# Kernel tuning notes

Measured on AMD Instinct MI355X. Metric: run time of the kernel, lower is better.

## Reference

```python
import jax, jax.numpy as jnp
import numpy as np

B, S, T = 128, 2048, 128


def setup_inputs() -> dict:
    key = jax.random.key(0)
    k1, k2, k3, k4, k5, k6 = jax.random.split(key, 6)
    logit = jax.random.normal(k1, (B, S, T), jnp.float32)
    target = jax.random.randint(k2, (B, S), 0, T, dtype=jnp.int32)
    seq_lens = jax.random.randint(k3, (B,), 1, S + 1, dtype=jnp.int32)
    transitions = 0.1 * jax.random.normal(k4, (T, T), jnp.float32)
    start_transitions = 0.1 * jax.random.normal(k5, (T,), jnp.float32)
    end_transitions = 0.1 * jax.random.normal(k6, (T,), jnp.float32)
    return dict(logit=logit, target=target, seq_lens=seq_lens,
                transitions=transitions, start_transitions=start_transitions,
                end_transitions=end_transitions)


def reference(logit, target, seq_lens, transitions, start_transitions, end_transitions):
    # logit: [B,S,T] batch-first; CRF works time-first like the torch code's transpose(0,1)
    em = jnp.transpose(logit, (1, 0, 2))          # [S,B,T]
    tg = target.T                                  # [S,B]
    mask = jnp.arange(S)[:, None] < seq_lens[None, :]  # [S,B]

    # ---- loss: -mean log-likelihood (CRF forward algorithm) ----
    emit = jnp.take_along_axis(em, tg[..., None], -1)[..., 0]   # [S,B]
    trans_sc = transitions[tg[:-1], tg[1:]]                      # [S-1,B]
    num = start_transitions[tg[0]] + emit[0]
    num = num + jnp.sum(jnp.where(mask[1:], emit[1:] + trans_sc, 0.0), axis=0)
    last_tags = jnp.take_along_axis(tg, (seq_lens - 1)[None, :], 0)[0]  # [B]
    num = num + end_transitions[last_tags]

    def fstep(alpha, xs):
        e_t, m_t = xs  # [B,T], [B]
        nxt = jax.nn.logsumexp(alpha[:, :, None] + transitions[None] + e_t[:, None, :], axis=1)
        return jnp.where(m_t[:, None], nxt, alpha), None

    alpha0 = start_transitions[None, :] + em[0]   # [B,T]
    alpha, _ = jax.lax.scan(fstep, alpha0, (em[1:], mask[1:]))
    logZ = jax.nn.logsumexp(alpha + end_transitions[None, :], axis=-1)  # [B]
    loss = -(num - logZ).mean()

    # ---- Viterbi decode ----
    tag_ids = jnp.arange(T, dtype=jnp.int32)

    def vstep(score, xs):
        e_t, m_t = xs
        mat = score[:, :, None] + transitions[None] + e_t[:, None, :]  # [B,Tprev,Tcur]
        best = mat.max(axis=1)
        idx = mat.argmax(axis=1).astype(jnp.int32)
        score = jnp.where(m_t[:, None], best, score)
        idx = jnp.where(m_t[:, None], idx, tag_ids[None, :])  # identity beyond seq end
        return score, idx

    vscore, hist = jax.lax.scan(vstep, alpha0, (em[1:], mask[1:]))  # hist: [S-1,B,T]
    last_tag = jnp.argmax(vscore + end_transitions[None, :], axis=-1).astype(jnp.int32)

    def bstep(tag, idx_t):
        prev = jnp.take_along_axis(idx_t, tag[:, None], 1)[:, 0]
        return prev, prev

    _, tags_prev = jax.lax.scan(bstep, last_tag, hist, reverse=True)  # [S-1,B]
    pred = jnp.concatenate([tags_prev, last_tag[None, :]], axis=0).T  # [B,S]

    # ---- _rearrange_output: swap decoded-tag logit with the max logit ----
    maxidx = jnp.argmax(logit, axis=-1)                         # [B,S]
    maxval = jnp.max(logit, axis=-1)                            # [B,S]
    vval = jnp.take_along_axis(logit, pred[..., None], -1)[..., 0]  # [B,S]
    oh_v = pred[..., None] == tag_ids[None, None, :]
    oh_m = maxidx[..., None] == tag_ids[None, None, :]
    swapped = jnp.where(oh_v, maxval[..., None],
                        jnp.where(oh_m, vval[..., None], logit))
    log_probs = jax.nn.log_softmax(swapped, axis=-1)            # [B,S,T]

    return loss, pred, log_probs
```

## Files before the change

kernel.cpp:

```cpp
#include <hip/hip_runtime.h>
#include <stdint.h>

#define BB 128
#define SS 2048
#define TT 128
#define NSEG 32
#define SEGK 64

#define TRP 129
#define VSTRIDE 136
#define H1OFF 68

typedef float f32x4 __attribute__((ext_vector_type(4)));

#define BAR() asm volatile("s_waitcnt lgkmcnt(0)\n\ts_barrier" ::: "memory")

#define PIN(x) asm volatile("" : "+v"(x))

__device__ __forceinline__ float dpp_swap1_f(float x) {
    int i = __float_as_int(x);
    i = __builtin_amdgcn_update_dpp(0, i, 0xB1, 0xF, 0xF, true);
    return __int_as_float(i);
}
__device__ __forceinline__ int dpp_swap1_i(int x) {
    return __builtin_amdgcn_update_dpp(0, x, 0xB1, 0xF, 0xF, true);
}

__attribute__((amdgpu_flat_work_group_size(256, 256)))
__attribute__((amdgpu_waves_per_eu(1, 1)))
__global__ void crf_mainX(const float* __restrict__ logit,
                          const int* __restrict__ seq_lens,
                          const float* __restrict__ trans,
                          const float* __restrict__ startT,
                          const float* __restrict__ endT,
                          const int* __restrict__ target,
                          uint8_t* __restrict__ histG,
                          float* __restrict__ scr_logZ,
                          int* __restrict__ scr_last,
                          float* __restrict__ scr_num)
{
    extern __shared__ float smem[];
    float* transLDS = smem;
    float* vecLDS   = smem + 16512;
    float* ringLDS  = smem + 16512 + 272;
    float* redLDS   = smem + 16512 + 276;
    int*   redILDS  = (int*)(smem + 16512 + 284);
    float* sumLDS   = smem + 16512 + 288;

    const int bid = blockIdx.x;
    const int role = bid >> 7;
    const int b = bid & (BB - 1);
    const int tid = threadIdx.x;
    const int j = tid >> 1;
    const int h = tid & 1;
    const int ibase0 = h << 6;
    const int joff = j + ((j >= 64) ? (H1OFF - 64) : 0);
    const int L = seq_lens[b];
    const size_t lbase = (size_t)b * (SS * TT);

    for (int m = tid; m < TT * TT; m += 256)
        transLDS[(m >> 7) * TRP + (m & 127)] = trans[m];
    __syncthreads();

    float e1 = 0.f, e2 = 0.f, e3 = 0.f;
    if (L > 1) e1 = logit[lbase + TT + j];
    e2 = (L > 2) ? logit[lbase + 2 * (size_t)TT + j] : e1;
    e3 = (L > 3) ? logit[lbase + 3 * (size_t)TT + j] : e2;

    if (role == 0) {
        f32x4 tC[16];
#pragma unroll
        for (int c = 0; c < 16; ++c) {
            tC[c].x = transLDS[(ibase0 + c * 4 + 0) * TRP + j];
            tC[c].y = transLDS[(ibase0 + c * 4 + 1) * TRP + j];
            tC[c].z = transLDS[(ibase0 + c * 4 + 2) * TRP + j];
            tC[c].w = transLDS[(ibase0 + c * 4 + 3) * TRP + j];
            PIN(tC[c]);
        }
        const float a0 = startT[j] + logit[lbase + j];
        if (h == 0) vecLDS[joff] = a0;
        __syncthreads();

        for (int t = 1; t < L; ++t) {
            const int cur = (t - 1) & 1, nxt = t & 1;
            const float e = e1; e1 = e2; e2 = e3;
            const int tn = (t + 3 < L) ? (t + 3) : (L - 1);
            e3 = logit[lbase + (size_t)tn * TT + j];

            const f32x4* sq = (const f32x4*)(vecLDS + cur * VSTRIDE + h * H1OFF);
            float cm[8];
#pragma unroll
            for (int c = 0; c < 8; ++c) {
                f32x4 pa = sq[2 * c] + tC[2 * c];
                f32x4 pb = sq[2 * c + 1] + tC[2 * c + 1];
                float m01 = fmaxf(pa.x, pa.y), m23 = fmaxf(pa.z, pa.w);
                float m45 = fmaxf(pb.x, pb.y), m67 = fmaxf(pb.z, pb.w);
                cm[c] = fmaxf(fmaxf(m01, m23), fmaxf(m45, m67));
            }
            float M = fmaxf(fmaxf(fmaxf(cm[0], cm[1]), fmaxf(cm[2], cm[3])),
                            fmaxf(fmaxf(cm[4], cm[5]), fmaxf(cm[6], cm[7])));
            const float Mall = fmaxf(M, dpp_swap1_f(M));
            const float v = Mall + e;

            int cwin = -1;
#pragma unroll
            for (int c = 7; c >= 0; --c) cwin = ((cm[c] + e) == v) ? c : cwin;

            int idx = 0x7fffffff;
            if (cwin >= 0) {
                const int basei = ibase0 + cwin * 8;
                const float* tr = transLDS + (size_t)basei * TRP + j;
                const f32x4* sr = (const f32x4*)(vecLDS + cur * VSTRIDE + h * H1OFF + cwin * 8);
                f32x4 ra = sr[0], rb = sr[1];
                float q0 = (ra.x + tr[0 * TRP]) + e;
                float q1 = (ra.y + tr[1 * TRP]) + e;
                float q2 = (ra.z + tr[2 * TRP]) + e;
                float q3 = (ra.w + tr[3 * TRP]) + e;
                float q4 = (rb.x + tr[4 * TRP]) + e;
                float q5 = (rb.y + tr[5 * TRP]) + e;
                float q6 = (rb.z + tr[6 * TRP]) + e;
                float q7 = (rb.w + tr[7 * TRP]) + e;
                idx = (q7 == v) ? basei + 7 : idx;
                idx = (q6 == v) ? basei + 6 : idx;
                idx = (q5 == v) ? basei + 5 : idx;
                idx = (q4 == v) ? basei + 4 : idx;
                idx = (q3 == v) ? basei + 3 : idx;
                idx = (q2 == v) ? basei + 2 : idx;
                idx = (q1 == v) ? basei + 1 : idx;
                idx = (q0 == v) ? basei + 0 : idx;
            }
            const int oidx = dpp_swap1_i(idx);
            idx = (oidx < idx) ? oidx : idx;

            if (h == 0) {
                vecLDS[nxt * VSTRIDE + joff] = v;
                histG[(size_t)b * (SS * TT) + (size_t)t * TT + j] = (uint8_t)idx;
            }
            BAR();
        }

        const int fin = (L - 1) & 1;
        if (tid < 128) {
            const int toff = tid + ((tid >= 64) ? (H1OFF - 64) : 0);
            float lv = vecLDS[fin * VSTRIDE + toff] + endT[tid];
            int li = tid;
#pragma unroll
            for (int off = 1; off < 64; off <<= 1) {
                float ov = __shfl_xor(lv, off);
                int oi = __shfl_xor(li, off);
                if (ov > lv || (ov == lv && oi < li)) { lv = ov; li = oi; }
            }
            if ((tid & 63) == 0) { redLDS[tid >> 6] = lv; redILDS[tid >> 6] = li; }
        }
        __syncthreads();
        if (tid == 0) {
            int lt = (redLDS[1] > redLDS[0] ||
                      (redLDS[1] == redLDS[0] && redILDS[1] < redILDS[0]))
                     ? redILDS[1] : redILDS[0];
            scr_last[b] = lt;
        }
        uint8_t* hb = histG + (size_t)b * (SS * TT);
        const int colq = (tid & 7) * 16;
        const uint32_t w0 = 0x03020100u + 0x01010101u * (uint32_t)colq;
        const uint4 pat = make_uint4(w0, w0 + 0x04040404u, w0 + 0x08080808u, w0 + 0x0C0C0C0Cu);
        for (int t0 = L; t0 < SS; t0 += 32) {
            int t = t0 + (tid >> 3);
            if (t < SS) *(uint4*)(hb + (size_t)t * TT + colq) = pat;
        }
    } else {
        f32x4 tE[16];
#pragma unroll
        for (int c = 0; c < 16; ++c) {
            tE[c].x = __expf(transLDS[(ibase0 + c * 4 + 0) * TRP + j]);
            tE[c].y = __expf(transLDS[(ibase0 + c * 4 + 1) * TRP + j]);
            tE[c].z = __expf(transLDS[(ibase0 + c * 4 + 2) * TRP + j]);
            tE[c].w = __expf(transLDS[(ibase0 + c * 4 + 3) * TRP + j]);
            PIN(tE[c]);
        }
        const float a0 = startT[j] + logit[lbase + j];
        const float R0 = startT[0] + logit[lbase + 0];
        float alpha = a0;
        if (h == 0) vecLDS[joff] = __expf(a0 - R0);
        if (tid < 4) ringLDS[tid] = R0;
        __syncthreads();

        for (int t = 1; t < L; ++t) {
            const int cur = (t - 1) & 1, nxt = t & 1;
            const float Rcons = ringLDS[(t - 3) & 3];
            const float Rpub  = ringLDS[(t - 2) & 3];
            const float e = e1; e1 = e2; e2 = e3;
            const int tn = (t + 3 < L) ? (t + 3) : (L - 1);
            e3 = logit[lbase + (size_t)tn * TT + j];

            const f32x4* aq = (const f32x4*)(vecLDS + cur * VSTRIDE + h * H1OFF);
            f32x4 s4 = {0.f, 0.f, 0.f, 0.f};
            f32x4 s4b = {0.f, 0.f, 0.f, 0.f};
#pragma unroll
            for (int c = 0; c < 16; c += 2) {
                s4  = aq[c] * tE[c] + s4;
                s4b = aq[c + 1] * tE[c + 1] + s4b;
            }
            f32x4 st = s4 + s4b;
            float Ssum = (st.x + st.y) + (st.z + st.w);
            Ssum += dpp_swap1_f(Ssum);
            alpha = e + Rcons + __logf(Ssum);
            const float p = __expf(alpha - Rpub);
            if (h == 0) vecLDS[nxt * VSTRIDE + joff] = p;
            if (tid == 0) ringLDS[t & 3] = alpha;
            BAR();
        }

        const float fval = alpha + endT[j];
        float tmx = fval;
#pragma unroll
        for (int off = 1; off < 64; off <<= 1) tmx = fmaxf(tmx, __shfl_xor(tmx, off));
        if ((tid & 63) == 0) redLDS[4 + (tid >> 6)] = tmx;
        __syncthreads();
        const float gm = fmaxf(fmaxf(redLDS[4], redLDS[5]), fmaxf(redLDS[6], redLDS[7]));
        float se = (h == 0) ? __expf(fval - gm) : 0.f;
#pragma unroll
        for (int off = 1; off < 64; off <<= 1) se += __shfl_xor(se, off);
        if ((tid & 63) == 0) sumLDS[tid >> 6] = se;
        __syncthreads();
        if (tid == 0)
            scr_logZ[b] = gm + __logf(sumLDS[0] + sumLDS[1] + sumLDS[2] + sumLDS[3]);
        __syncthreads();

        float acc = 0.f;
        for (int t = tid; t < L; t += 256) {
            int tg = target[b * SS + t];
            acc += logit[((size_t)b * SS + t) * TT + tg];
            if (t >= 1) acc += trans[target[b * SS + t - 1] * TT + tg];
        }
#pragma unroll
        for (int off = 1; off < 64; off <<= 1) acc += __shfl_xor(acc, off);
        if ((tid & 63) == 0) sumLDS[tid >> 6] = acc;
        __syncthreads();
        if (tid == 0) {
            float tot = sumLDS[0] + sumLDS[1] + sumLDS[2] + sumLDS[3];
            tot += startT[target[b * SS]] + endT[target[b * SS + L - 1]];
            scr_num[b] = tot;
        }
    }
}

__global__ void crf_btseg(uint8_t* __restrict__ histG)
{
    const int c = blockIdx.x;
    const int b = blockIdx.y;
    const int tid = threadIdx.x;
    __shared__ __align__(16) uint8_t hl[SEGK * TT];

    const int lo = (c == 0) ? 1 : c * SEGK;
    const int nr = (c == 0) ? 63 : 64;
    const uint8_t* src = histG + (size_t)b * (SS * TT) + (size_t)lo * TT;
    for (int k = tid; k < (nr * TT) / 16; k += 128)
        ((uint4*)hl)[k] = ((const uint4*)src)[k];
    __syncthreads();

    int tau = tid;
    uint32_t w[16];
#pragma unroll
    for (int q = 0; q < 16; ++q) w[q] = 0u;
    if (c == 0) {
#pragma unroll
        for (int r = 62; r >= 0; --r) {
            tau = hl[r * TT + tau];
            w[r >> 2] |= ((uint32_t)tau) << ((r & 3) * 8);
        }
    } else {
#pragma unroll
        for (int r = 63; r >= 0; --r) {
            tau = hl[r * TT + tau];
            w[r >> 2] |= ((uint32_t)tau) << ((r & 3) * 8);
        }
    }
    uint4* dst = (uint4*)(histG + (size_t)b * (SS * TT) + (size_t)c * 8192 + (size_t)tid * 64);
    dst[0] = make_uint4(w[0], w[1], w[2], w[3]);
    dst[1] = make_uint4(w[4], w[5], w[6], w[7]);
    dst[2] = make_uint4(w[8], w[9], w[10], w[11]);
    dst[3] = make_uint4(w[12], w[13], w[14], w[15]);
}

__global__ void crf_btchain(const uint8_t* __restrict__ histG,
                            const int* __restrict__ scr_last,
                            int* __restrict__ scr_bt,
                            float* __restrict__ out_pred)
{
    const int b = threadIdx.x;
    if (b >= BB) return;
    int tau = scr_last[b];
    out_pred[(size_t)b * SS + (SS - 1)] = (float)tau;
    for (int c = NSEG - 1; c >= 0; --c) {
        scr_bt[b * NSEG + c] = tau;
        tau = histG[(size_t)b * (SS * TT) + (size_t)c * 8192 + (size_t)tau * 64];
    }
}

__global__ void crf_btfill(const uint8_t* __restrict__ histG,
                           const int* __restrict__ scr_bt,
                           float* __restrict__ out_pred)
{
    const int c = blockIdx.x;
    const int b = blockIdx.y;
    const int s = threadIdx.x;
    if (c == 0 && s > 62) return;
    const int js = scr_bt[b * NSEG + c];
    uint8_t v = histG[(size_t)b * (SS * TT) + (size_t)c * 8192 + (size_t)js * 64 + s];
    const int pos = (c == 0) ? s : (c * SEGK - 1 + s);
    out_pred[(size_t)b * SS + pos] = (float)v;
}

__global__ void crf_loss(const float* __restrict__ scr_logZ, const float* __restrict__ scr_num,
                         float* __restrict__ out)
{
    const int tid = threadIdx.x;
    __shared__ float p2[2];
    float v = (tid < BB) ? (scr_logZ[tid] - scr_num[tid]) : 0.0f;
#pragma unroll
    for (int off = 1; off < 64; off <<= 1) v += __shfl_xor(v, off);
    if ((tid & 63) == 0) p2[tid >> 6] = v;
    __syncthreads();
    if (tid == 0) out[0] = (p2[0] + p2[1]) / (float)BB;
}

__global__ void crf_logprobs(const float* __restrict__ logit,
                             const float* __restrict__ predF,
                             float* __restrict__ outLP)
{
    const int wid = threadIdx.x >> 6;
    const int lane = threadIdx.x & 63;
    const size_t row = (size_t)blockIdx.x * 4 + wid;
    const float2* rp = (const float2*)(logit + row * TT);
    float2 v = rp[lane];
    const int pred = (int)predF[row];

    float mv; int mi;
    if (v.y > v.x) { mv = v.y; mi = lane * 2 + 1; }
    else           { mv = v.x; mi = lane * 2; }
#pragma unroll
    for (int off = 1; off < 64; off <<= 1) {
        float ov = __shfl_xor(mv, off);
        int oi = __shfl_xor(mi, off);
        if (ov > mv || (ov == mv && oi < mi)) { mv = ov; mi = oi; }
    }
    float se = __expf(v.x - mv) + __expf(v.y - mv);
#pragma unroll
    for (int off = 1; off < 64; off <<= 1) se += __shfl_xor(se, off);
    const float lse = __logf(se);

    float px = __shfl(v.x, pred >> 1);
    float py = __shfl(v.y, pred >> 1);
    float vp = (pred & 1) ? py : px;

    float ox = (lane * 2 == pred) ? mv : ((lane * 2 == mi) ? vp : v.x);
    float oy = (lane * 2 + 1 == pred) ? mv : ((lane * 2 + 1 == mi) ? vp : v.y);
    float* op = outLP + row * TT + lane * 2;
    op[0] = (ox - mv) - lse;
    op[1] = (oy - mv) - lse;
}

extern "C" void kernel_launch(void* const* d_in, const int* in_sizes, int n_in,
                              void* d_out, int out_size, void* d_ws, size_t ws_size,
                              hipStream_t stream)
{
    const float* logit    = (const float*)d_in[0];
    const int*   target   = (const int*)d_in[1];
    const int*   seq_lens = (const int*)d_in[2];
    const float* trans    = (const float*)d_in[3];
    const float* startT   = (const float*)d_in[4];
    const float* endT     = (const float*)d_in[5];

    float* out      = (float*)d_out;
    float* out_pred = out + 1;
    float* outLP    = out + 1 + (size_t)BB * SS;
    uint8_t* histG  = (uint8_t*)(out + 262148);
    float* scr      = out + ((size_t)1 + (size_t)BB * SS + (size_t)BB * SS * TT - 4480);
    float* scr_logZ = scr;
    float* scr_num  = scr + 128;
    int*   scr_last = (int*)(scr + 256);
    int*   scr_bt   = (int*)(scr + 384);

    const int dynLDS = (16512 + 272 + 4 + 8 + 4 + 4 + 8) * 4;
    hipFuncSetAttribute((const void*)crf_mainX,
                        hipFuncAttributeMaxDynamicSharedMemorySize, dynLDS);

    crf_mainX<<<2 * BB, 256, dynLDS, stream>>>(logit, seq_lens, trans, startT, endT,
                                               target, histG, scr_logZ, scr_last, scr_num);
    crf_btseg<<<dim3(NSEG, BB), 128, 0, stream>>>(histG);
    crf_btchain<<<1, 128, 0, stream>>>(histG, scr_last, scr_bt, out_pred);
    crf_btfill<<<dim3(NSEG, BB), 64, 0, stream>>>(histG, scr_bt, out_pred);
    crf_loss<<<1, 128, 0, stream>>>(scr_logZ, scr_num, out);
    crf_logprobs<<<(BB * SS) / 4, 256, 0, stream>>>(logit, out_pred, outLP);
}
```

Measured before the change: 1.591 ms.

## Remap CRF recurrence threads to 4 outputs x 8 input groups per lane

Changes the thread mapping in the forward and Viterbi recurrences. Each lane now computes 4 output tags over a 16-wide slice of previous tags, where before it handled one tag over half the inputs. The 8-lane reduction uses three DPP steps, and emissions, state writes and history bytes move as 4-wide vectors. The goal is to cut LDS state reads per step and vectorize the global accesses, at the cost of a longer DPP reduction chain per step and a new padded state layout.

```diff
diff --git a/kernel.cpp b/kernel.cpp
--- a/kernel.cpp
+++ b/kernel.cpp
@@ -8,22 +8,28 @@
 #define SEGK 64
 
 #define TRP 129
-#define VSTRIDE 136
-#define H1OFF 68
+#define SPITCH 160
+#define PI(i) ((i) + (((i) >> 4) << 2))
 
 typedef float f32x4 __attribute__((ext_vector_type(4)));
 
 #define BAR() asm volatile("s_waitcnt lgkmcnt(0)\n\ts_barrier" ::: "memory")
-
 #define PIN(x) asm volatile("" : "+v"(x))
 
-__device__ __forceinline__ float dpp_swap1_f(float x) {
-    int i = __float_as_int(x);
-    i = __builtin_amdgcn_update_dpp(0, i, 0xB1, 0xF, 0xF, true);
-    return __int_as_float(i);
-}
-__device__ __forceinline__ int dpp_swap1_i(int x) {
-    return __builtin_amdgcn_update_dpp(0, x, 0xB1, 0xF, 0xF, true);
+template <int CTRL>
+__device__ __forceinline__ float dppf(float x) {
+    return __int_as_float(__builtin_amdgcn_update_dpp(0, __float_as_int(x), CTRL, 0xF, 0xF, true));
+}
+template <int CTRL>
+__device__ __forceinline__ int dppi(int x) {
+    return __builtin_amdgcn_update_dpp(0, x, CTRL, 0xF, 0xF, true);
+}
+
+__device__ __forceinline__ f32x4 fmax4(f32x4 a, f32x4 b) {
+    f32x4 r;
+    r.x = fmaxf(a.x, b.x); r.y = fmaxf(a.y, b.y);
+    r.z = fmaxf(a.z, b.z); r.w = fmaxf(a.w, b.w);
+    return r;
 }
 
 __attribute__((amdgpu_flat_work_group_size(256, 256)))
@@ -41,20 +47,22 @@
 {
     extern __shared__ float smem[];
     float* transLDS = smem;
-    float* vecLDS   = smem + 16512;
-    float* ringLDS  = smem + 16512 + 272;
-    float* redLDS   = smem + 16512 + 276;
-    int*   redILDS  = (int*)(smem + 16512 + 284);
-    float* sumLDS   = smem + 16512 + 288;
-
-    const int bid = blockIdx.x;
+    float* stateLDS = smem + 16512;
+    float* ringLDS  = smem + 16832;
+    float* redLDS   = smem + 16836;
+    int*   redILDS  = (int*)(smem + 16844);
+    float* sumLDS   = smem + 16848;
+
+    const int bid  = blockIdx.x;
     const int role = bid >> 7;
-    const int b = bid & (BB - 1);
-    const int tid = threadIdx.x;
-    const int j = tid >> 1;
-    const int h = tid & 1;
-    const int ibase0 = h << 6;
-    const int joff = j + ((j >= 64) ? (H1OFF - 64) : 0);
+    const int b    = bid & (BB - 1);
+    const int tid  = threadIdx.x;
+    const int w    = tid >> 6;
+    const int lane = tid & 63;
+    const int ig   = lane & 7;
+    const int jd   = lane >> 3;
+    const int j0   = w * 32 + jd * 4;
+    const int ibase = ig * 16;
     const int L = seq_lens[b];
     const size_t lbase = (size_t)b * (SS * TT);
 
@@ -62,87 +70,89 @@
         transLDS[(m >> 7) * TRP + (m & 127)] = trans[m];
     __syncthreads();
 
-    float e1 = 0.f, e2 = 0.f, e3 = 0.f;
-    if (L > 1) e1 = logit[lbase + TT + j];
-    e2 = (L > 2) ? logit[lbase + 2 * (size_t)TT + j] : e1;
-    e3 = (L > 3) ? logit[lbase + 3 * (size_t)TT + j] : e2;
+    f32x4 e1 = {0,0,0,0}, e2, e3;
+    if (L > 1) e1 = *(const f32x4*)(logit + lbase + (size_t)TT + j0);
+    e2 = (L > 2) ? *(const f32x4*)(logit + lbase + 2 * (size_t)TT + j0) : e1;
+    e3 = (L > 3) ? *(const f32x4*)(logit + lbase + 3 * (size_t)TT + j0) : e2;
+
+    const f32x4 st4 = *(const f32x4*)(startT + j0);
+    const f32x4 l04 = *(const f32x4*)(logit + lbase + j0);
+    const f32x4 a04 = st4 + l04;
 
     if (role == 0) {
-        f32x4 tC[16];
-#pragma unroll
-        for (int c = 0; c < 16; ++c) {
-            tC[c].x = transLDS[(ibase0 + c * 4 + 0) * TRP + j];
-            tC[c].y = transLDS[(ibase0 + c * 4 + 1) * TRP + j];
-            tC[c].z = transLDS[(ibase0 + c * 4 + 2) * TRP + j];
-            tC[c].w = transLDS[(ibase0 + c * 4 + 3) * TRP + j];
-            PIN(tC[c]);
-        }
-        const float a0 = startT[j] + logit[lbase + j];
-        if (h == 0) vecLDS[joff] = a0;
-        __syncthreads();
+        f32x4 tj[4][4];
+#pragma unroll
+        for (int q = 0; q < 4; ++q)
+#pragma unroll
+            for (int c = 0; c < 4; ++c) {
+                tj[q][c].x = transLDS[(ibase + c * 4 + 0) * TRP + (j0 + q)];
+                tj[q][c].y = transLDS[(ibase + c * 4 + 1) * TRP + (j0 + q)];
+                tj[q][c].z = transLDS[(ibase + c * 4 + 2) * TRP + (j0 + q)];
+                tj[q][c].w = transLDS[(ibase + c * 4 + 3) * TRP + (j0 + q)];
+                PIN(tj[q][c]);
+            }
+        if (ig == 0) *(f32x4*)(stateLDS + PI(j0)) = a04;
+        __syncthreads();
+
+        uint8_t* hb = histG + (size_t)b * (SS * TT);
 
         for (int t = 1; t < L; ++t) {
             const int cur = (t - 1) & 1, nxt = t & 1;
-            const float e = e1; e1 = e2; e2 = e3;
+            const f32x4 e4 = e1; e1 = e2; e2 = e3;
             const int tn = (t + 3 < L) ? (t + 3) : (L - 1);
-            e3 = logit[lbase + (size_t)tn * TT + j];
-
-            const f32x4* sq = (const f32x4*)(vecLDS + cur * VSTRIDE + h * H1OFF);
-            float cm[8];
-#pragma unroll
-            for (int c = 0; c < 8; ++c) {
-                f32x4 pa = sq[2 * c] + tC[2 * c];
-                f32x4 pb = sq[2 * c + 1] + tC[2 * c + 1];
-                float m01 = fmaxf(pa.x, pa.y), m23 = fmaxf(pa.z, pa.w);
-                float m45 = fmaxf(pb.x, pb.y), m67 = fmaxf(pb.z, pb.w);
-                cm[c] = fmaxf(fmaxf(m01, m23), fmaxf(m45, m67));
-            }
-            float M = fmaxf(fmaxf(fmaxf(cm[0], cm[1]), fmaxf(cm[2], cm[3])),
-                            fmaxf(fmaxf(cm[4], cm[5]), fmaxf(cm[6], cm[7])));
-            const float Mall = fmaxf(M, dpp_swap1_f(M));
-            const float v = Mall + e;
-
-            int cwin = -1;
-#pragma unroll
-            for (int c = 7; c >= 0; --c) cwin = ((cm[c] + e) == v) ? c : cwin;
-
-            int idx = 0x7fffffff;
-            if (cwin >= 0) {
-                const int basei = ibase0 + cwin * 8;
-                const float* tr = transLDS + (size_t)basei * TRP + j;
-                const f32x4* sr = (const f32x4*)(vecLDS + cur * VSTRIDE + h * H1OFF + cwin * 8);
-                f32x4 ra = sr[0], rb = sr[1];
-                float q0 = (ra.x + tr[0 * TRP]) + e;
-                float q1 = (ra.y + tr[1 * TRP]) + e;
-                float q2 = (ra.z + tr[2 * TRP]) + e;
-                float q3 = (ra.w + tr[3 * TRP]) + e;
-                float q4 = (rb.x + tr[4 * TRP]) + e;
-                float q5 = (rb.y + tr[5 * TRP]) + e;
-                float q6 = (rb.z + tr[6 * TRP]) + e;
-                float q7 = (rb.w + tr[7 * TRP]) + e;
-                idx = (q7 == v) ? basei + 7 : idx;
-                idx = (q6 == v) ? basei + 6 : idx;
-                idx = (q5 == v) ? basei + 5 : idx;
-                idx = (q4 == v) ? basei + 4 : idx;
-                idx = (q3 == v) ? basei + 3 : idx;
-                idx = (q2 == v) ? basei + 2 : idx;
-                idx = (q1 == v) ? basei + 1 : idx;
-                idx = (q0 == v) ? basei + 0 : idx;
-            }
-            const int oidx = dpp_swap1_i(idx);
-            idx = (oidx < idx) ? oidx : idx;
-
-            if (h == 0) {
-                vecLDS[nxt * VSTRIDE + joff] = v;
-                histG[(size_t)b * (SS * TT) + (size_t)t * TT + j] = (uint8_t)idx;
+            e3 = *(const f32x4*)(logit + lbase + (size_t)tn * TT + j0);
+
+            const f32x4* sq = (const f32x4*)(stateLDS + cur * SPITCH + 20 * ig);
+            f32x4 s0 = sq[0], s1 = sq[1], s2 = sq[2], s3 = sq[3];
+
+            float va[4];
+            int   pidx[4];
+#pragma unroll
+            for (int q = 0; q < 4; ++q) {
+                f32x4 P[4];
+                P[0] = s0 + tj[q][0];
+                P[1] = s1 + tj[q][1];
+                P[2] = s2 + tj[q][2];
+                P[3] = s3 + tj[q][3];
+                f32x4 m4 = fmax4(fmax4(P[0], P[1]), fmax4(P[2], P[3]));
+                float M = fmaxf(fmaxf(m4.x, m4.y), fmaxf(m4.z, m4.w));
+                M = fmaxf(M, dppf<0xB1>(M));
+                M = fmaxf(M, dppf<0x4E>(M));
+                M = fmaxf(M, dppf<0x141>(M));
+                const float e = (q == 0) ? e4.x : (q == 1) ? e4.y : (q == 2) ? e4.z : e4.w;
+                const float v = M + e;
+                int idx = 0x7fffffff;
+                const f32x4 esp = {e, e, e, e};
+#pragma unroll
+                for (int c = 3; c >= 0; --c) {
+                    f32x4 qv = P[c] + esp;
+                    idx = (qv.w == v) ? (ibase + c * 4 + 3) : idx;
+                    idx = (qv.z == v) ? (ibase + c * 4 + 2) : idx;
+                    idx = (qv.y == v) ? (ibase + c * 4 + 1) : idx;
+                    idx = (qv.x == v) ? (ibase + c * 4 + 0) : idx;
+                }
+                int o;
+                o = dppi<0xB1>(idx);  idx = (o < idx) ? o : idx;
+                o = dppi<0x4E>(idx);  idx = (o < idx) ? o : idx;
+                o = dppi<0x141>(idx); idx = (o < idx) ? o : idx;
+                va[q] = v;
+                pidx[q] = idx;
+            }
+            if (ig == 0) {
+                f32x4 vv = {va[0], va[1], va[2], va[3]};
+                *(f32x4*)(stateLDS + nxt * SPITCH + PI(j0)) = vv;
+            }
+            if (ig == 1) {
+                uint32_t pk = (uint32_t)pidx[0] | ((uint32_t)pidx[1] << 8) |
+                              ((uint32_t)pidx[2] << 16) | ((uint32_t)pidx[3] << 24);
+                *(uint32_t*)(hb + (size_t)t * TT + j0) = pk;
             }
             BAR();
         }
 
         const int fin = (L - 1) & 1;
         if (tid < 128) {
-            const int toff = tid + ((tid >= 64) ? (H1OFF - 64) : 0);
-            float lv = vecLDS[fin * VSTRIDE + toff] + endT[tid];
+            float lv = stateLDS[fin * SPITCH + PI(tid)] + endT[tid];
             int li = tid;
 #pragma unroll
             for (int off = 1; off < 64; off <<= 1) {
@@ -159,7 +169,6 @@
                      ? redILDS[1] : redILDS[0];
             scr_last[b] = lt;
         }
-        uint8_t* hb = histG + (size_t)b * (SS * TT);
         const int colq = (tid & 7) * 16;
         const uint32_t w0 = 0x03020100u + 0x01010101u * (uint32_t)colq;
         const uint4 pat = make_uint4(w0, w0 + 0x04040404u, w0 + 0x08080808u, w0 + 0x0C0C0C0Cu);
@@ -168,19 +177,24 @@
             if (t < SS) *(uint4*)(hb + (size_t)t * TT + colq) = pat;
         }
     } else {
-        f32x4 tE[16];
-#pragma unroll
-        for (int c = 0; c < 16; ++c) {
-            tE[c].x = __expf(transLDS[(ibase0 + c * 4 + 0) * TRP + j]);
-            tE[c].y = __expf(transLDS[(ibase0 + c * 4 + 1) * TRP + j]);
-            tE[c].z = __expf(transLDS[(ibase0 + c * 4 + 2) * TRP + j]);
-            tE[c].w = __expf(transLDS[(ibase0 + c * 4 + 3) * TRP + j]);
-            PIN(tE[c]);
-        }
-        const float a0 = startT[j] + logit[lbase + j];
-        const float R0 = startT[0] + logit[lbase + 0];
-        float alpha = a0;
-        if (h == 0) vecLDS[joff] = __expf(a0 - R0);
+        f32x4 tE[4][4];
+#pragma unroll
+        for (int q = 0; q < 4; ++q)
+#pragma unroll
+            for (int c = 0; c < 4; ++c) {
+                tE[q][c].x = __expf(transLDS[(ibase + c * 4 + 0) * TRP + (j0 + q)]);
+                tE[q][c].y = __expf(transLDS[(ibase + c * 4 + 1) * TRP + (j0 + q)]);
+                tE[q][c].z = __expf(transLDS[(ibase + c * 4 + 2) * TRP + (j0 + q)]);
+                tE[q][c].w = __expf(transLDS[(ibase + c * 4 + 3) * TRP + (j0 + q)]);
+                PIN(tE[q][c]);
+            }
+        const float R0 = startT[0] + logit[lbase];
+        float aa[4] = {a04.x, a04.y, a04.z, a04.w};
+        if (ig == 0) {
+            f32x4 ex = {__expf(a04.x - R0), __expf(a04.y - R0),
+                        __expf(a04.z - R0), __expf(a04.w - R0)};
+            *(f32x4*)(stateLDS + PI(j0)) = ex;
+        }
         if (tid < 4) ringLDS[tid] = R0;
         __syncthreads();
 
@@ -188,36 +202,52 @@
             const int cur = (t - 1) & 1, nxt = t & 1;
             const float Rcons = ringLDS[(t - 3) & 3];
             const float Rpub  = ringLDS[(t - 2) & 3];
-            const float e = e1; e1 = e2; e2 = e3;
+            const f32x4 e4 = e1; e1 = e2; e2 = e3;
             const int tn = (t + 3 < L) ? (t + 3) : (L - 1);
-            e3 = logit[lbase + (size_t)tn * TT + j];
-
-            const f32x4* aq = (const f32x4*)(vecLDS + cur * VSTRIDE + h * H1OFF);
-            f32x4 s4 = {0.f, 0.f, 0.f, 0.f};
-            f32x4 s4b = {0.f, 0.f, 0.f, 0.f};
-#pragma unroll
-            for (int c = 0; c < 16; c += 2) {
-                s4  = aq[c] * tE[c] + s4;
-                s4b = aq[c + 1] * tE[c + 1] + s4b;
-            }
-            f32x4 st = s4 + s4b;
-            float Ssum = (st.x + st.y) + (st.z + st.w);
-            Ssum += dpp_swap1_f(Ssum);
-            alpha = e + Rcons + __logf(Ssum);
-            const float p = __expf(alpha - Rpub);
-            if (h == 0) vecLDS[nxt * VSTRIDE + joff] = p;
-            if (tid == 0) ringLDS[t & 3] = alpha;
+            e3 = *(const f32x4*)(logit + lbase + (size_t)tn * TT + j0);
+
+            const f32x4* aq = (const f32x4*)(stateLDS + cur * SPITCH + 20 * ig);
+            f32x4 s0 = aq[0], s1 = aq[1], s2 = aq[2], s3 = aq[3];
+
+            float pv[4];
+#pragma unroll
+            for (int q = 0; q < 4; ++q) {
+                f32x4 acc = s0 * tE[q][0];
+                acc = s1 * tE[q][1] + acc;
+                acc = s2 * tE[q][2] + acc;
+                acc = s3 * tE[q][3] + acc;
+                float S = (acc.x + acc.y) + (acc.z + acc.w);
+                S += dppf<0xB1>(S);
+                S += dppf<0x4E>(S);
+                S += dppf<0x141>(S);
+                const float e = (q == 0) ? e4.x : (q == 1) ? e4.y : (q == 2) ? e4.z : e4.w;
+                const float alpha = e + Rcons + __logf(S);
+                aa[q] = alpha;
+                pv[q] = __expf(alpha - Rpub);
+            }
+            if (ig == 0) {
+                f32x4 pp = {pv[0], pv[1], pv[2], pv[3]};
+                *(f32x4*)(stateLDS + nxt * SPITCH + PI(j0)) = pp;
+            }
+            if (tid == 0) ringLDS[t & 3] = aa[0];
             BAR();
         }
 
-        const float fval = alpha + endT[j];
+        const int freeb = L & 1;
+        if (ig == 0) {
+            f32x4 av = {aa[0], aa[1], aa[2], aa[3]};
+            *(f32x4*)(stateLDS + freeb * SPITCH + PI(j0)) = av;
+        }
+        __syncthreads();
+        float fval = -3.4e38f;
+        if (tid < 128) fval = stateLDS[freeb * SPITCH + PI(tid)] + endT[tid];
         float tmx = fval;
 #pragma unroll
         for (int off = 1; off < 64; off <<= 1) tmx = fmaxf(tmx, __shfl_xor(tmx, off));
         if ((tid & 63) == 0) redLDS[4 + (tid >> 6)] = tmx;
         __syncthreads();
-        const float gm = fmaxf(fmaxf(redLDS[4], redLDS[5]), fmaxf(redLDS[6], redLDS[7]));
-        float se = (h == 0) ? __expf(fval - gm) : 0.f;
+        const float gm = fmaxf(redLDS[4], redLDS[5]);
+        float se = (tid < 128) ? __expf(fval - gm) : 0.f;
 #pragma unroll
         for (int off = 1; off < 64; off <<= 1) se += __shfl_xor(se, off);
         if ((tid & 63) == 0) sumLDS[tid >> 6] = se;
@@ -381,7 +411,7 @@
     int*   scr_last = (int*)(scr + 256);
     int*   scr_bt   = (int*)(scr + 384);
 
-    const int dynLDS = (16512 + 272 + 4 + 8 + 4 + 4 + 8) * 4;
+    const int dynLDS = 16852 * 4;
     hipFuncSetAttribute((const void*)crf_mainX,
                         hipFuncAttributeMaxDynamicSharedMemorySize, dynLDS);
 
```

Measured after the change: 1.883 ms. 18.4% more time.
